# Optimization experiments

Measured on AMD Instinct MI355X. Metric: run time of the kernel, lower is better.

The kernel has to match this reference:

```python
import jax, jax.numpy as jnp
import numpy as np


def setup_inputs() -> dict:
    key = jax.random.key(0)
    k1, k2, k3, k4, k5 = jax.random.split(key, 5)
    B, T, U, D, H, V = 4, 256, 96, 512, 512, 1024
    return {
        "encoder_outputs": jax.random.normal(k1, (B, T, D), dtype=jnp.float32),
        "decoder_outputs": jax.random.normal(k2, (B, U, D), dtype=jnp.float32),
        # W1: torch Linear(input_size=2D -> H) weight, stored here as (2D, H)
        "W1": jax.random.normal(k3, (2 * D, H), dtype=jnp.float32) * 0.02,
        "b1": jax.random.normal(k4, (H,), dtype=jnp.float32) * 0.02,
        # W2: torch Linear(H -> V, bias=False) weight, stored as (H, V)
        "W2": jax.random.normal(k5, (H, V), dtype=jnp.float32) * 0.02,
    }


def reference(encoder_outputs, decoder_outputs, W1, b1, W2):
    # Faithful to: repeat/cat to (B,T,U,2D) -> Linear -> GELU(tanh) -> Linear.
    # concat-then-Linear == split W1 into enc/dec halves and broadcast-add,
    # which avoids materializing the (B,T,U,2D) tensor (same math exactly).
    D = encoder_outputs.shape[-1]
    We, Wd = W1[:D], W1[D:]                      # (D,H), (D,H)
    he = jnp.einsum("btd,dh->bth", encoder_outputs, We)   # (B,T,H)
    hd = jnp.einsum("bud,dh->buh", decoder_outputs, Wd)   # (B,U,H)
    h = he[:, :, None, :] + hd[:, None, :, :] + b1         # (B,T,U,H)
    h = jax.nn.gelu(h, approximate=True)                   # tanh GELU
    return jnp.einsum("btuh,hv->btuv", h, W2)              # (B,T,U,V)
```

## Files before the change

### kernel.cpp

```cpp
#include <hip/hip_runtime.h>
#include <hip/hip_bf16.h>

typedef __attribute__((ext_vector_type(8))) short short8;
typedef __attribute__((ext_vector_type(4))) float f32x4;

__device__ __forceinline__ unsigned short f2bf(float f) {
    union { __hip_bfloat16 h; unsigned short u; } cv;
    cv.h = __float2bfloat16(f);
    return cv.u;
}

__device__ __forceinline__ float gelu_t(float x) {
    float e = __expf(1.5957691216057308f * x * __builtin_fmaf(0.044715f, x * x, 1.0f));
    return x * (e / (e + 1.0f));
}

__device__ __forceinline__ void gload_lds16(const void* g, void* l) {
    __builtin_amdgcn_global_load_lds((const __attribute__((address_space(1))) unsigned int*)g,
                                     (__attribute__((address_space(3))) unsigned int*)l, 16, 0, 0);
}

__device__ __forceinline__ int swzkey(int r) { return ((r >> 1) & 3) << 4; }

__global__ __launch_bounds__(256) void transpose_all(const float* __restrict__ W1,
                                                     const float* __restrict__ W2,
                                                     unsigned short* __restrict__ Wet,
                                                     unsigned short* __restrict__ Wdt,
                                                     unsigned short* __restrict__ W2t) {
    int z = blockIdx.z;
    if (z < 2 && blockIdx.y >= 8) return;
    const float* in = (z == 0) ? W1 : (z == 1) ? (W1 + 512 * 512) : W2;
    unsigned short* out = (z == 0) ? Wet : (z == 1) ? Wdt : W2t;
    int N = (z == 2) ? 1024 : 512;

    __shared__ float tile[64][65];
    int k0 = blockIdx.x * 64, n0 = blockIdx.y * 64;
    int t = threadIdx.x;
    int c = t & 63, r0 = t >> 6;
#pragma unroll
    for (int i = 0; i < 16; i++) {
        int r = r0 + i * 4;
        tile[r][c] = in[(size_t)(k0 + r) * N + n0 + c];
    }
    __syncthreads();
    int kk = t & 15;
    int nl0 = t >> 4;
#pragma unroll
    for (int i = 0; i < 4; i++) {
        int nl = nl0 + i * 16;
        int n  = n0 + nl;
        unsigned short b0 = f2bf(tile[kk * 4 + 0][nl]);
        unsigned short b1 = f2bf(tile[kk * 4 + 1][nl]);
        unsigned short b2 = f2bf(tile[kk * 4 + 2][nl]);
        unsigned short b3 = f2bf(tile[kk * 4 + 3][nl]);
        uint2 v;
        v.x = (unsigned)b0 | ((unsigned)b1 << 16);
        v.y = (unsigned)b2 | ((unsigned)b3 << 16);
        int byte_in_chunk = kk * 8;
        int slice = byte_in_chunk & ~63;
        int off   = (byte_in_chunk & 63) ^ swzkey(n);
        size_t obyte = (size_t)n * 1024 + (size_t)k0 * 2 + slice + off;
        *(uint2*)((char*)out + obyte) = v;
    }
}

__global__ __launch_bounds__(256, 2) void gemm_small(const float* __restrict__ enc,
                                                     const float* __restrict__ dec,
                                                     const unsigned short* __restrict__ Wet,
                                                     const unsigned short* __restrict__ Wdt,
                                                     const float* __restrict__ b1,
                                                     float* __restrict__ he,
                                                     float* __restrict__ hd) {
    bool isEnc = blockIdx.x < 8;
    const float* A = isEnc ? enc : dec;
    const unsigned short* Bt = isEnc ? Wet : Wdt;
    const float* bias = isEnc ? b1 : nullptr;
    float* C = isEnc ? he : hd;
    size_t m0 = (size_t)(isEnc ? blockIdx.x : blockIdx.x - 8) * 128;

    __shared__ alignas(16) unsigned short As[128 * 32];
    __shared__ alignas(16) unsigned short Bs[128 * 32];
    int t = threadIdx.x;
    int n0 = blockIdx.y * 128;
    int lane = t & 63, w = t >> 6;
    int wm = w >> 1, wn = w & 1;
    int rA = t >> 3, cg = t & 7;
    f32x4 acc[4][4] = {};

    for (int kt = 0; kt < 16; ++kt) {
        int k0 = kt * 32;
        __syncthreads();
#pragma unroll
        for (int p = 0; p < 4; p++) {
            int r = rA + p * 32;
            f32x4 v = *(const f32x4*)&A[(m0 + r) * 512 + k0 + cg * 4];
            uint2 pk;
            pk.x = (unsigned)f2bf(v.x) | ((unsigned)f2bf(v.y) << 16);
            pk.y = (unsigned)f2bf(v.z) | ((unsigned)f2bf(v.w) << 16);
            int off = (cg * 8) ^ swzkey(r);
            *(uint2*)((char*)As + r * 64 + off) = pk;
        }
#pragma unroll
        for (int j = 0; j < 2; j++) {
            int ibyte = w * 1024 + j * 4096;
            int lb = ibyte + lane * 16;
            int row = lb >> 6, colb = lb & 63;
            const char* src = (const char*)Bt + (size_t)(n0 + row) * 1024 + k0 * 2 + colb;
            gload_lds16(src, (char*)Bs + ibyte);
        }
        __syncthreads();
        short8 af[4], bf[4];
#pragma unroll
        for (int mi = 0; mi < 4; mi++) {
            int r = wm * 64 + mi * 16 + (lane & 15);
            int off = ((lane >> 4) * 16) ^ swzkey(r);
            af[mi] = *(const short8*)((const char*)As + r * 64 + off);
        }
#pragma unroll
        for (int ni = 0; ni < 4; ni++) {
            int n = wn * 64 + ni * 16 + (lane & 15);
            int off = ((lane >> 4) * 16) ^ swzkey(n);
            bf[ni] = *(const short8*)((const char*)Bs + n * 64 + off);
        }
#pragma unroll
        for (int mi = 0; mi < 4; mi++)
#pragma unroll
            for (int ni = 0; ni < 4; ni++)
                acc[mi][ni] = __builtin_amdgcn_mfma_f32_16x16x32_bf16(af[mi], bf[ni], acc[mi][ni], 0, 0, 0);
    }
#pragma unroll
    for (int mi = 0; mi < 4; mi++) {
        int row = wm * 64 + mi * 16 + ((lane >> 4) << 2);
#pragma unroll
        for (int ni = 0; ni < 4; ni++) {
            int col = n0 + wn * 64 + ni * 16 + (lane & 15);
            float bv = bias ? bias[col] : 0.0f;
#pragma unroll
            for (int q = 0; q < 4; q++)
                C[(m0 + row + q) * 512 + col] = acc[mi][ni][q] + bv;
        }
    }
}

__global__ __launch_bounds__(512, 4) void joint_fused(const float* __restrict__ he,
                                                      const float* __restrict__ hd,
                                                      const unsigned short* __restrict__ W2t,
                                                      float* __restrict__ out) {
    __shared__ alignas(16) char lds[73728];
    int t = threadIdx.x;
    int lane = t & 63, w = t >> 6;
    int wm = w >> 2, wn = w & 3;
    int bx = blockIdx.x;
    int mt = (bx & 7) * 192 + (bx >> 3);
    size_t m0 = (size_t)mt * 64;
    int n0 = blockIdx.y * 512;

    int rA = t >> 3, cg = t & 7;
    int mrow = (int)m0 + rA;
    int tI = mrow / 96;
    int u  = mrow - tI * 96;
    const float* eP = he + (size_t)tI * 512 + cg * 4;
    const float* dP = hd + (size_t)((tI >> 8) * 96 + u) * 512 + cg * 4;
    int aoff = rA * 64 + ((cg * 8) ^ swzkey(rA));

    const char* bSrc[4];
#pragma unroll
    for (int i = 0; i < 4; i++) {
        int row = w * 64 + i * 16 + (lane >> 2);
        bSrc[i] = (const char*)W2t + (size_t)(n0 + row) * 1024 + (lane & 3) * 16;
    }

    int l15 = lane & 15, lg = lane >> 4;
    int aOff[2], bOff[8];
#pragma unroll
    for (int mi = 0; mi < 2; mi++) {
        int r = wm * 32 + mi * 16 + l15;
        aOff[mi] = r * 64 + ((lg * 16) ^ swzkey(r));
    }
#pragma unroll
    for (int ni = 0; ni < 8; ni++) {
        int n = wn * 128 + ni * 16 + l15;
        bOff[ni] = 8192 + n * 64 + ((lg * 16) ^ swzkey(n));
    }

    f32x4 acc[2][8] = {};
    f32x4 er[2], dr[2];

#define LOADED(slot, kt)  do { \
        er[slot] = *(const f32x4*)(eP + (kt) * 32); \
        dr[slot] = *(const f32x4*)(dP + (kt) * 32); } while (0)

#define STAGE_B(buf, kt)  do { \
        _Pragma("unroll") \
        for (int i = 0; i < 4; i++) \
            gload_lds16(bSrc[i] + (kt) * 64, lds + 8192 + (buf) * 32768 + w * 4096 + i * 1024); } while (0)

#define GELU_A(buf, slot) do { \
        uint2 pk; \
        pk.x = (unsigned)f2bf(gelu_t(er[slot].x + dr[slot].x)) | \
               ((unsigned)f2bf(gelu_t(er[slot].y + dr[slot].y)) << 16); \
        pk.y = (unsigned)f2bf(gelu_t(er[slot].z + dr[slot].z)) | \
               ((unsigned)f2bf(gelu_t(er[slot].w + dr[slot].w)) << 16); \
        *(uint2*)(lds + (buf) * 4096 + aoff) = pk; } while (0)

    STAGE_B(0, 0);
    LOADED(0, 0);
    LOADED(1, 1);
    GELU_A(0, 0);
    asm volatile("s_waitcnt lgkmcnt(0)" ::: "memory");
    asm volatile("s_waitcnt vmcnt(2)" ::: "memory");
    __builtin_amdgcn_sched_barrier(0);
    __builtin_amdgcn_s_barrier();
    __builtin_amdgcn_sched_barrier(0);

#pragma unroll
    for (int kt = 0; kt < 16; ++kt) {
        const int cur = kt & 1, nxt = cur ^ 1;
        if (kt < 15) STAGE_B(nxt, kt + 1);
        if (kt < 14) LOADED(cur, kt + 2);
        if (kt < 15) GELU_A(nxt, nxt);
        short8 a[2];
#pragma unroll
        for (int mi = 0; mi < 2; mi++) a[mi] = *(const short8*)(lds + cur * 4096 + aOff[mi]);
        __builtin_amdgcn_s_setprio(1);
#pragma unroll
        for (int ni = 0; ni < 8; ni++) {
            short8 b = *(const short8*)(lds + cur * 32768 + bOff[ni]);
#pragma unroll
            for (int mi = 0; mi < 2; mi++)
                acc[mi][ni] = __builtin_amdgcn_mfma_f32_16x16x32_bf16(a[mi], b, acc[mi][ni], 0, 0, 0);
        }
        __builtin_amdgcn_s_setprio(0);
        if (kt < 15) {
            asm volatile("s_waitcnt lgkmcnt(0)" ::: "memory");
            __builtin_amdgcn_sched_barrier(0);
            if (kt < 14) asm volatile("s_waitcnt vmcnt(2)" ::: "memory");
            else         asm volatile("s_waitcnt vmcnt(0)" ::: "memory");
            __builtin_amdgcn_sched_barrier(0);
            __builtin_amdgcn_s_barrier();
            __builtin_amdgcn_sched_barrier(0);
        }
    }
#undef LOADED
#undef STAGE_B
#undef GELU_A

    asm volatile("s_waitcnt lgkmcnt(0)" ::: "memory");
    __builtin_amdgcn_sched_barrier(0);
    __builtin_amdgcn_s_barrier();
    __builtin_amdgcn_sched_barrier(0);

    char* ep = lds + w * 8448;
    int l31 = lane & 31, lh = lane >> 5;
#pragma unroll
    for (int mi = 0; mi < 2; mi++) {
#pragma unroll
        for (int ni = 0; ni < 8; ni++) {
            int c = ni * 16 + l15;
#pragma unroll
            for (int q = 0; q < 4; q++)
                *(float*)(ep + ((lg * 4 + q) * 132 + c) * 4) = acc[mi][ni][q];
        }
        asm volatile("s_waitcnt lgkmcnt(0)" ::: "memory");
        __builtin_amdgcn_sched_barrier(0);
#pragma unroll
        for (int it = 0; it < 8; it++) {
            int r = it * 2 + lh;
            f32x4 v = *(const f32x4*)(ep + (r * 132 + l31 * 4) * 4);
            size_t row = m0 + wm * 32 + mi * 16 + r;
            float* o = out + row * 1024 + n0 + wn * 128 + l31 * 4;
            __builtin_nontemporal_store(v, (f32x4*)o);
        }
        asm volatile("s_waitcnt lgkmcnt(0)" ::: "memory");
        __builtin_amdgcn_sched_barrier(0);
    }
}

extern "C" void kernel_launch(void* const* d_in, const int* in_sizes, int n_in,
                              void* d_out, int out_size, void* d_ws, size_t ws_size,
                              hipStream_t stream) {
    const float* enc = (const float*)d_in[0];
    const float* dec = (const float*)d_in[1];
    const float* W1  = (const float*)d_in[2];
    const float* b1  = (const float*)d_in[3];
    const float* W2  = (const float*)d_in[4];
    float* out = (float*)d_out;

    char* ws = (char*)d_ws;
    float* he = (float*)(ws);
    float* hd = (float*)(ws + 2097152);
    unsigned short* Wet = (unsigned short*)(ws + 2883584);
    unsigned short* Wdt = (unsigned short*)(ws + 3407872);
    unsigned short* W2t = (unsigned short*)(ws + 3932160);

    transpose_all<<<dim3(8, 16, 3), 256, 0, stream>>>(W1, W2, Wet, Wdt, W2t);
    gemm_small<<<dim3(11, 4), 256, 0, stream>>>(enc, dec, Wet, Wdt, b1, he, hd);
    joint_fused<<<dim3(1536, 2), 512, 0, stream>>>(he, hd, W2t, out);
}
```

Measured before the change: 193.2 us.

## Retile joint GEMM to 256x256 blocks with K=64 steps and interleaved GELU staging

Changes the fused joint kernel from 64x512 tiles to 256x256 tiles, with each warp computing a 128x64 sub-tile over K=64 steps in double-buffered 128KB LDS. GELU generation and B staging for the next step are interleaved between MFMA groups to hide latency. The aim is to cut repeated GELU work on A across N tiles and raise MFMA arithmetic intensity. The cost is occupancy dropping to one block per CU and higher register pressure from 32 accumulators.

```diff
diff --git a/kernel.cpp b/kernel.cpp
--- a/kernel.cpp
+++ b/kernel.cpp
@@ -142,133 +142,168 @@
     }
 }
 
-__global__ __launch_bounds__(512, 4) void joint_fused(const float* __restrict__ he,
+__global__ __launch_bounds__(512, 1) void joint_fused(const float* __restrict__ he,
                                                       const float* __restrict__ hd,
                                                       const unsigned short* __restrict__ W2t,
                                                       float* __restrict__ out) {
-    __shared__ alignas(16) char lds[73728];
+    __shared__ alignas(16) char lds[131072];
+    constexpr int BB = 65536;
     int t = threadIdx.x;
     int lane = t & 63, w = t >> 6;
     int wm = w >> 2, wn = w & 3;
     int bx = blockIdx.x;
-    int mt = (bx & 7) * 192 + (bx >> 3);
-    size_t m0 = (size_t)mt * 64;
-    int n0 = blockIdx.y * 512;
-
-    int rA = t >> 3, cg = t & 7;
-    int mrow = (int)m0 + rA;
-    int tI = mrow / 96;
-    int u  = mrow - tI * 96;
-    const float* eP = he + (size_t)tI * 512 + cg * 4;
-    const float* dP = hd + (size_t)((tI >> 8) * 96 + u) * 512 + cg * 4;
-    int aoff = rA * 64 + ((cg * 8) ^ swzkey(rA));
-
-    const char* bSrc[4];
-#pragma unroll
-    for (int i = 0; i < 4; i++) {
-        int row = w * 64 + i * 16 + (lane >> 2);
-        bSrc[i] = (const char*)W2t + (size_t)(n0 + row) * 1024 + (lane & 3) * 16;
-    }
-
+    int mt = (bx & 7) * 48 + (bx >> 3);
+    size_t m0 = (size_t)mt * 256;
+    int n0 = blockIdx.y * 256;
+
+    int rT = t >> 3, cg = t & 7;
+    const float* eP[4];
+    const float* dP[4];
+    int aw[4];
+#pragma unroll
+    for (int p = 0; p < 4; p++) {
+        int r = rT + p * 64;
+        int mrow = (int)m0 + r;
+        int tI = mrow / 96, u = mrow - tI * 96;
+        eP[p] = he + (size_t)tI * 512 + cg * 8;
+        dP[p] = hd + (size_t)((tI >> 8) * 96 + u) * 512 + cg * 8;
+        aw[p] = (cg >> 2) * 16384 + r * 64 + (((cg & 3) * 16) ^ swzkey(r));
+    }
+    const char* bsrc[4];
+#pragma unroll
+    for (int j = 0; j < 4; j++) {
+        int nl = (w & 3) * 64 + j * 16 + (lane >> 2);
+        bsrc[j] = (const char*)W2t + (size_t)(n0 + nl) * 1024 + (w >> 2) * 64 + (lane & 3) * 16;
+    }
     int l15 = lane & 15, lg = lane >> 4;
-    int aOff[2], bOff[8];
-#pragma unroll
-    for (int mi = 0; mi < 2; mi++) {
-        int r = wm * 32 + mi * 16 + l15;
-        aOff[mi] = r * 64 + ((lg * 16) ^ swzkey(r));
-    }
-#pragma unroll
-    for (int ni = 0; ni < 8; ni++) {
-        int n = wn * 128 + ni * 16 + l15;
-        bOff[ni] = 8192 + n * 64 + ((lg * 16) ^ swzkey(n));
-    }
-
-    f32x4 acc[2][8] = {};
-    f32x4 er[2], dr[2];
-
-#define LOADED(slot, kt)  do { \
-        er[slot] = *(const f32x4*)(eP + (kt) * 32); \
-        dr[slot] = *(const f32x4*)(dP + (kt) * 32); } while (0)
-
-#define STAGE_B(buf, kt)  do { \
-        _Pragma("unroll") \
-        for (int i = 0; i < 4; i++) \
-            gload_lds16(bSrc[i] + (kt) * 64, lds + 8192 + (buf) * 32768 + w * 4096 + i * 1024); } while (0)
-
-#define GELU_A(buf, slot) do { \
-        uint2 pk; \
-        pk.x = (unsigned)f2bf(gelu_t(er[slot].x + dr[slot].x)) | \
-               ((unsigned)f2bf(gelu_t(er[slot].y + dr[slot].y)) << 16); \
-        pk.y = (unsigned)f2bf(gelu_t(er[slot].z + dr[slot].z)) | \
-               ((unsigned)f2bf(gelu_t(er[slot].w + dr[slot].w)) << 16); \
-        *(uint2*)(lds + (buf) * 4096 + aoff) = pk; } while (0)
-
-    STAGE_B(0, 0);
-    LOADED(0, 0);
-    LOADED(1, 1);
-    GELU_A(0, 0);
+    int aO[8], bO[4];
+#pragma unroll
+    for (int mi = 0; mi < 8; mi++) {
+        int r = wm * 128 + mi * 16 + l15;
+        aO[mi] = r * 64 + ((lg * 16) ^ swzkey(r));
+    }
+#pragma unroll
+    for (int ni = 0; ni < 4; ni++) {
+        int n = wn * 64 + ni * 16 + l15;
+        bO[ni] = n * 64 + ((lg * 16) ^ swzkey(n));
+    }
+
+    f32x4 acc[8][4] = {};
+    f32x4 se0, se1, sd0, sd1;
+
+#define HL(p, t1)  do { \
+        se0 = *(const f32x4*)(eP[p] + (t1) * 64); \
+        se1 = *(const f32x4*)(eP[p] + (t1) * 64 + 4); \
+        sd0 = *(const f32x4*)(dP[p] + (t1) * 64); \
+        sd1 = *(const f32x4*)(dP[p] + (t1) * 64 + 4); } while (0)
+
+#define GEN(p, buf) do { uint4 pk; \
+        pk.x = (unsigned)f2bf(gelu_t(se0.x + sd0.x)) | ((unsigned)f2bf(gelu_t(se0.y + sd0.y)) << 16); \
+        pk.y = (unsigned)f2bf(gelu_t(se0.z + sd0.z)) | ((unsigned)f2bf(gelu_t(se0.w + sd0.w)) << 16); \
+        pk.z = (unsigned)f2bf(gelu_t(se1.x + sd1.x)) | ((unsigned)f2bf(gelu_t(se1.y + sd1.y)) << 16); \
+        pk.w = (unsigned)f2bf(gelu_t(se1.z + sd1.z)) | ((unsigned)f2bf(gelu_t(se1.w + sd1.w)) << 16); \
+        *(uint4*)(lds + (buf) * 32768 + aw[p]) = pk; } while (0)
+
+#define STAGE(buf, t1, j) \
+        gload_lds16(bsrc[j] + (size_t)(t1) * 128, lds + BB + (buf) * 32768 + w * 4096 + (j) * 1024)
+
+    STAGE(0, 0, 0); STAGE(0, 0, 1); STAGE(0, 0, 2); STAGE(0, 0, 3);
+    HL(0, 0); GEN(0, 0);
+    HL(1, 0); GEN(1, 0);
+    HL(2, 0); GEN(2, 0);
+    HL(3, 0); GEN(3, 0);
     asm volatile("s_waitcnt lgkmcnt(0)" ::: "memory");
-    asm volatile("s_waitcnt vmcnt(2)" ::: "memory");
+    asm volatile("s_waitcnt vmcnt(0)" ::: "memory");
     __builtin_amdgcn_sched_barrier(0);
     __builtin_amdgcn_s_barrier();
     __builtin_amdgcn_sched_barrier(0);
 
 #pragma unroll
-    for (int kt = 0; kt < 16; ++kt) {
-        const int cur = kt & 1, nxt = cur ^ 1;
-        if (kt < 15) STAGE_B(nxt, kt + 1);
-        if (kt < 14) LOADED(cur, kt + 2);
-        if (kt < 15) GELU_A(nxt, nxt);
-        short8 a[2];
-#pragma unroll
-        for (int mi = 0; mi < 2; mi++) a[mi] = *(const short8*)(lds + cur * 4096 + aOff[mi]);
+    for (int tt = 0; tt < 8; ++tt) {
+        const int cur = tt & 1, nxt = cur ^ 1;
+        const char* Ab = lds + cur * 32768;
+        const char* Bb = lds + BB + cur * 32768;
+        const bool pre = (tt < 7);
+        short8 a[8], b0, b1, b2, b3;
+        if (pre) { STAGE(nxt, tt + 1, 0); STAGE(nxt, tt + 1, 1); HL(0, tt + 1); }
+#pragma unroll
+        for (int mi = 0; mi < 8; mi++) a[mi] = *(const short8*)(Ab + aO[mi]);
+        b0 = *(const short8*)(Bb + bO[0]);
+        b1 = *(const short8*)(Bb + bO[1]);
         __builtin_amdgcn_s_setprio(1);
 #pragma unroll
-        for (int ni = 0; ni < 8; ni++) {
-            short8 b = *(const short8*)(lds + cur * 32768 + bOff[ni]);
-#pragma unroll
-            for (int mi = 0; mi < 2; mi++)
-                acc[mi][ni] = __builtin_amdgcn_mfma_f32_16x16x32_bf16(a[mi], b, acc[mi][ni], 0, 0, 0);
+        for (int mi = 0; mi < 8; mi++) {
+            acc[mi][0] = __builtin_amdgcn_mfma_f32_16x16x32_bf16(a[mi], b0, acc[mi][0], 0, 0, 0);
+            acc[mi][1] = __builtin_amdgcn_mfma_f32_16x16x32_bf16(a[mi], b1, acc[mi][1], 0, 0, 0);
         }
         __builtin_amdgcn_s_setprio(0);
-        if (kt < 15) {
+        if (pre) { GEN(0, nxt); HL(1, tt + 1); }
+        b2 = *(const short8*)(Bb + bO[2]);
+        b3 = *(const short8*)(Bb + bO[3]);
+        __builtin_amdgcn_s_setprio(1);
+#pragma unroll
+        for (int mi = 0; mi < 8; mi++) {
+            acc[mi][2] = __builtin_amdgcn_mfma_f32_16x16x32_bf16(a[mi], b2, acc[mi][2], 0, 0, 0);
+            acc[mi][3] = __builtin_amdgcn_mfma_f32_16x16x32_bf16(a[mi], b3, acc[mi][3], 0, 0, 0);
+        }
+        __builtin_amdgcn_s_setprio(0);
+        if (pre) { STAGE(nxt, tt + 1, 2); STAGE(nxt, tt + 1, 3); GEN(1, nxt); HL(2, tt + 1); }
+#pragma unroll
+        for (int mi = 0; mi < 8; mi++) a[mi] = *(const short8*)(Ab + 16384 + aO[mi]);
+        b0 = *(const short8*)(Bb + 16384 + bO[0]);
+        b1 = *(const short8*)(Bb + 16384 + bO[1]);
+        __builtin_amdgcn_s_setprio(1);
+#pragma unroll
+        for (int mi = 0; mi < 8; mi++) {
+            acc[mi][0] = __builtin_amdgcn_mfma_f32_16x16x32_bf16(a[mi], b0, acc[mi][0], 0, 0, 0);
+            acc[mi][1] = __builtin_amdgcn_mfma_f32_16x16x32_bf16(a[mi], b1, acc[mi][1], 0, 0, 0);
+        }
+        __builtin_amdgcn_s_setprio(0);
+        if (pre) { GEN(2, nxt); HL(3, tt + 1); }
+        b2 = *(const short8*)(Bb + 16384 + bO[2]);
+        b3 = *(const short8*)(Bb + 16384 + bO[3]);
+        __builtin_amdgcn_s_setprio(1);
+#pragma unroll
+        for (int mi = 0; mi < 8; mi++) {
+            acc[mi][2] = __builtin_amdgcn_mfma_f32_16x16x32_bf16(a[mi], b2, acc[mi][2], 0, 0, 0);
+            acc[mi][3] = __builtin_amdgcn_mfma_f32_16x16x32_bf16(a[mi], b3, acc[mi][3], 0, 0, 0);
+        }
+        __builtin_amdgcn_s_setprio(0);
+        if (pre) {
+            GEN(3, nxt);
             asm volatile("s_waitcnt lgkmcnt(0)" ::: "memory");
             __builtin_amdgcn_sched_barrier(0);
-            if (kt < 14) asm volatile("s_waitcnt vmcnt(2)" ::: "memory");
-            else         asm volatile("s_waitcnt vmcnt(0)" ::: "memory");
+            asm volatile("s_waitcnt vmcnt(0)" ::: "memory");
             __builtin_amdgcn_sched_barrier(0);
             __builtin_amdgcn_s_barrier();
             __builtin_amdgcn_sched_barrier(0);
         }
     }
-#undef LOADED
-#undef STAGE_B
-#undef GELU_A
+#undef HL
+#undef GEN
+#undef STAGE
 
     asm volatile("s_waitcnt lgkmcnt(0)" ::: "memory");
     __builtin_amdgcn_sched_barrier(0);
     __builtin_amdgcn_s_barrier();
     __builtin_amdgcn_sched_barrier(0);
 
-    char* ep = lds + w * 8448;
-    int l31 = lane & 31, lh = lane >> 5;
-#pragma unroll
-    for (int mi = 0; mi < 2; mi++) {
-#pragma unroll
-        for (int ni = 0; ni < 8; ni++) {
-            int c = ni * 16 + l15;
+    char* ep = lds + w * 4352;
+#pragma unroll
+    for (int mi = 0; mi < 8; mi++) {
+#pragma unroll
+        for (int ni = 0; ni < 4; ni++)
 #pragma unroll
             for (int q = 0; q < 4; q++)
-                *(float*)(ep + ((lg * 4 + q) * 132 + c) * 4) = acc[mi][ni][q];
-        }
+                *(float*)(ep + (lg * 4 + q) * 272 + (ni * 16 + l15) * 4) = acc[mi][ni][q];
         asm volatile("s_waitcnt lgkmcnt(0)" ::: "memory");
         __builtin_amdgcn_sched_barrier(0);
 #pragma unroll
-        for (int it = 0; it < 8; it++) {
-            int r = it * 2 + lh;
-            f32x4 v = *(const f32x4*)(ep + (r * 132 + l31 * 4) * 4);
-            size_t row = m0 + wm * 32 + mi * 16 + r;
-            float* o = out + row * 1024 + n0 + wn * 128 + l31 * 4;
+        for (int it = 0; it < 4; it++) {
+            int r = it * 4 + lg;
+            f32x4 v = *(const f32x4*)(ep + r * 272 + l15 * 16);
+            size_t row = m0 + wm * 128 + mi * 16 + r;
+            float* o = out + row * 1024 + n0 + wn * 64 + l15 * 4;
             __builtin_nontemporal_store(v, (f32x4*)o);
         }
         asm volatile("s_waitcnt lgkmcnt(0)" ::: "memory");
@@ -295,5 +330,5 @@
 
     transpose_all<<<dim3(8, 16, 3), 256, 0, stream>>>(W1, W2, Wet, Wdt, W2t);
     gemm_small<<<dim3(11, 4), 256, 0, stream>>>(enc, dec, Wet, Wdt, b1, he, hd);
-    joint_fused<<<dim3(1536, 2), 512, 0, stream>>>(he, hd, W2t, out);
-}
+    joint_fused<<<dim3(384, 4), 512, 0, stream>>>(he, hd, W2t, out);
+}
```

Measured after the change: 257.6 us. 33.3% more time.
